# Performance work log

Measured on AMD Instinct MI355X. Metric: run time of the kernel, lower is better.

The kernel has to match this reference:

```python
import jax, jax.numpy as jnp
import numpy as np

B, T, C = 8, 1024, 1024
H, D = 16, 64  # num_heads, head_size

def setup_inputs() -> dict:
    key = jax.random.key(0)
    ks = jax.random.split(key, 6)
    s = C ** -0.5
    return {
        "x": jax.random.normal(ks[0], (B, T, C), dtype=jnp.float32),
        "Wq": jax.random.normal(ks[1], (H, C, D), dtype=jnp.float32) * s,
        "Wk": jax.random.normal(ks[2], (H, C, D), dtype=jnp.float32) * s,
        "Wv": jax.random.normal(ks[3], (H, C, D), dtype=jnp.float32) * s,
        "Wproj": jax.random.normal(ks[4], (H * D, C), dtype=jnp.float32) * ((H * D) ** -0.5),
        "bproj": jnp.zeros((C,), dtype=jnp.float32),
    }

def reference(x, Wq, Wk, Wv, Wproj, bproj):
    # per-head QKV projections, batched over heads via einsum (same math as looped heads)
    q = jnp.einsum('btc,hcd->bhtd', x, Wq)
    k = jnp.einsum('btc,hcd->bhtd', x, Wk)
    v = jnp.einsum('btc,hcd->bhtd', x, Wv)
    scale = D ** -0.5  # k.shape[-1]**-0.5 in original head
    scores = jnp.einsum('bhtd,bhsd->bhts', q, k) * scale  # [B,H,T,T]
    Tn = x.shape[1]
    causal = jnp.tril(jnp.ones((Tn, Tn), dtype=bool))
    scores = jnp.where(causal, scores, jnp.float32(-jnp.inf))
    att = jax.nn.softmax(scores, axis=-1)
    out = jnp.einsum('bhts,bhsd->bhtd', att, v)          # [B,H,T,D]
    out = out.transpose(0, 2, 1, 3).reshape(x.shape[0], Tn, H * D)  # concat heads
    return out @ Wproj + bproj  # dropout is identity at p=0.0
```

## Files before the change

### kernel.cpp

```cpp
#include <hip/hip_runtime.h>
#include <hip/hip_bf16.h>

#define B_ 8
#define T_ 1024
#define C_ 1024
#define H_ 16
#define D_ 64
#define QKVLD 3072

typedef short v4s __attribute__((ext_vector_type(4)));
typedef short v8s __attribute__((ext_vector_type(8)));
typedef float v4f __attribute__((ext_vector_type(4)));
typedef float v16f __attribute__((ext_vector_type(16)));

__device__ __forceinline__ unsigned short f2b(float f) {
    unsigned int u = __builtin_bit_cast(unsigned int, f);
    unsigned int lsb = (u >> 16) & 1u;
    u += 0x7fffu + lsb;
    return (unsigned short)(u >> 16);
}

__device__ __forceinline__ v4s pack4(float p0, float p1, float p2, float p3) {
    unsigned int a = (__builtin_bit_cast(unsigned int, p0) + 0x8000u) >> 16;
    unsigned int b = (__builtin_bit_cast(unsigned int, p1) + 0x8000u) & 0xFFFF0000u;
    unsigned int c = (__builtin_bit_cast(unsigned int, p2) + 0x8000u) >> 16;
    unsigned int d = (__builtin_bit_cast(unsigned int, p3) + 0x8000u) & 0xFFFF0000u;
    union { unsigned int u[2]; v4s v; } t;
    t.u[0] = a | b; t.u[1] = c | d;
    return t.v;
}

#define MFMA32(A, B, C) __builtin_amdgcn_mfma_f32_16x16x32_bf16(A, B, C, 0, 0, 0)
#define MFMA16(A, B, C) __builtin_amdgcn_mfma_f32_16x16x16bf16_1k(A, B, C, 0, 0, 0)

#define GLOAD16(gp, lp)                                                          \
    __builtin_amdgcn_global_load_lds(                                            \
        (const __attribute__((address_space(1))) unsigned int*)(gp),             \
        (__attribute__((address_space(3))) unsigned int*)(lp), 16, 0, 0)

__global__ void prep_kernel(const float* __restrict__ x, const float* __restrict__ Wq,
                            const float* __restrict__ Wk, const float* __restrict__ Wv,
                            const float* __restrict__ Wproj,
                            unsigned short* __restrict__ xb,
                            unsigned short* __restrict__ WqkvT,
                            unsigned short* __restrict__ WprojT) {
    __shared__ unsigned short t[64][65];
    int g = blockIdx.x;
    if (g < 8192) {
        int i = (g * 256 + (int)threadIdx.x) * 4;
        float4 v = *(const float4*)(x + i);
        ushort4 o;
        o.x = f2b(v.x); o.y = f2b(v.y); o.z = f2b(v.z); o.w = f2b(v.w);
        *(ushort4*)(xb + i) = o;
    } else if (g < 8192 + 768) {
        int idx = g - 8192;
        int z = idx >> 4;
        int h = z / 3, part = z % 3;
        const float* src = (part == 0 ? Wq : (part == 1 ? Wk : Wv)) + (size_t)h * C_ * D_;
        int c0 = (idx & 15) * 64;
        for (int i = threadIdx.x; i < 4096; i += 256) {
            int r = i >> 6, d = i & 63;
            t[d][r] = f2b(src[(size_t)(c0 + r) * D_ + d]);
        }
        __syncthreads();
        unsigned short* dst = WqkvT + (size_t)(part * 1024 + h * 64) * C_;
        for (int i = threadIdx.x; i < 4096; i += 256) {
            int d = i >> 6, r = i & 63;
            dst[(size_t)d * C_ + c0 + r] = t[d][r];
        }
    } else {
        int idx = g - 8960;
        int n0 = (idx & 15) * 64, k0 = (idx >> 4) * 64;
        for (int i = threadIdx.x; i < 4096; i += 256) {
            int r = i >> 6, c = i & 63;
            t[c][r] = f2b(Wproj[(size_t)(k0 + r) * C_ + n0 + c]);
        }
        __syncthreads();
        for (int i = threadIdx.x; i < 4096; i += 256) {
            int n = i >> 6, k = i & 63;
            WprojT[(size_t)(n0 + n) * 1024 + k0 + k] = t[n][k];
        }
    }
}

__global__ __launch_bounds__(256, 2) void gemm_qkv(const unsigned short* __restrict__ A,
                                                   const unsigned short* __restrict__ Bt,
                                                   unsigned short* __restrict__ Cout,
                                                   unsigned short* __restrict__ Vt,
                                                   int K, int ldc) {
    __shared__ unsigned short smem[24576];

    int tid = threadIdx.x;
    int lane = tid & 63, w = tid >> 6;
    int half = lane >> 5, l32 = lane & 31;
    int wm = w >> 1, wn = w & 1;
    int g = blockIdx.x;
    int xcd = g & 7;
    int bank = g >> 3;
    int j = g >> 4;

    if ((bank & 1) == 0) {
        constexpr int ABUF = 256 * 32;
        constexpr int BBUF = 128 * 32;
        unsigned short* lA0 = smem;
        unsigned short* lB0 = smem + 2 * ABUF;

        int m0 = (xcd * 4 + (j & 3)) * 256;
        int n0 = (j >> 2) * 128;

        const unsigned short* gA[4];
        int offA[4];
        #pragma unroll
        for (int jj = 0; jj < 4; jj++) {
            int c = jj * 256 + tid;
            int row = c >> 2;
            int col8 = ((c & 3) ^ ((row >> 1) & 3)) * 8;
            gA[jj] = A + (size_t)(m0 + row) * K + col8;
            offA[jj] = (jj * 256 + w * 64) * 16;
        }
        const unsigned short* gB[2];
        int offB[2];
        #pragma unroll
        for (int jj = 0; jj < 2; jj++) {
            int c = jj * 256 + tid;
            int row = c >> 2;
            int col8 = ((c & 3) ^ ((row >> 1) & 3)) * 8;
            gB[jj] = Bt + (size_t)(n0 + row) * K + col8;
            offB[jj] = (jj * 256 + w * 64) * 16;
        }

        int am[4], bn[2];
        #pragma unroll
        for (int mi = 0; mi < 4; mi++) am[mi] = wm * 128 + mi * 32 + l32;
        #pragma unroll
        for (int ni = 0; ni < 2; ni++) bn[ni] = wn * 64 + ni * 32 + l32;

        v16f acc[4][2];
        #pragma unroll
        for (int mi = 0; mi < 4; mi++)
            #pragma unroll
            for (int ni = 0; ni < 2; ni++)
                #pragma unroll
                for (int r = 0; r < 16; r++) acc[mi][ni][r] = 0.f;

        int ktiles = K >> 5;
        #pragma unroll
        for (int jj = 0; jj < 4; jj++) GLOAD16(gA[jj], (char*)lA0 + offA[jj]);
        #pragma unroll
        for (int jj = 0; jj < 2; jj++) GLOAD16(gB[jj], (char*)lB0 + offB[jj]);

        for (int it = 0; it < ktiles; it++) {
            int cur = it & 1, nxt = cur ^ 1;
            __asm__ volatile("s_waitcnt vmcnt(0)" ::: "memory");
            __asm__ volatile("s_barrier" ::: "memory");
            {
                int kn = (it + 1 < ktiles) ? (it + 1) * 32 : it * 32;
                #pragma unroll
                for (int jj = 0; jj < 4; jj++) GLOAD16(gA[jj] + kn, (char*)(lA0 + nxt * ABUF) + offA[jj]);
                #pragma unroll
                for (int jj = 0; jj < 2; jj++) GLOAD16(gB[jj] + kn, (char*)(lB0 + nxt * BBUF) + offB[jj]);
            }
            const unsigned short* bufA = lA0 + cur * ABUF;
            const unsigned short* bufB = lB0 + cur * BBUF;
            #pragma unroll
            for (int step = 0; step < 2; step++) {
                int gc = step * 2 + half;
                v8s af[4], bf[2];
                #pragma unroll
                for (int mi = 0; mi < 4; mi++)
                    af[mi] = *(const v8s*)&bufA[am[mi] * 32 + ((gc ^ ((am[mi] >> 1) & 3)) * 8)];
                #pragma unroll
                for (int ni = 0; ni < 2; ni++)
                    bf[ni] = *(const v8s*)&bufB[bn[ni] * 32 + ((gc ^ ((bn[ni] >> 1) & 3)) * 8)];
                #pragma unroll
                for (int mi = 0; mi < 4; mi++)
                    #pragma unroll
                    for (int ni = 0; ni < 2; ni++)
                        acc[mi][ni] = __builtin_amdgcn_mfma_f32_32x32x16_bf16(af[mi], bf[ni], acc[mi][ni], 0, 0, 0);
            }
        }
        float scl = (n0 >= 1024) ? 0.125f : 1.0f;
        #pragma unroll
        for (int mi = 0; mi < 4; mi++) {
            #pragma unroll
            for (int ni = 0; ni < 2; ni++) {
                int col = n0 + wn * 64 + ni * 32 + l32;
                #pragma unroll
                for (int r = 0; r < 16; r++) {
                    int row = m0 + wm * 128 + mi * 32 + (r & 3) + 8 * (r >> 2) + 4 * half;
                    Cout[(size_t)row * ldc + col] = f2b(acc[mi][ni][r] * scl);
                }
            }
        }
    } else {
        constexpr int ABUF = 128 * 32;
        constexpr int BBUF = 128 * 32;
        unsigned short* lA = smem;
        unsigned short* lB = smem + 3 * ABUF;

        const unsigned short* Bv = Bt + (size_t)2048 * K;
        int m0 = (xcd * 8 + (j & 7)) * 128;
        int n0 = (j >> 3) * 128;

        const unsigned short* gA[2];
        int offA[2];
        #pragma unroll
        for (int jj = 0; jj < 2; jj++) {
            int c = jj * 256 + tid;
            int row = c >> 2;
            int col8 = ((c & 3) ^ ((row >> 1) & 3)) * 8;
            gA[jj] = A + (size_t)(m0 + row) * K + col8;
            offA[jj] = (jj * 256 + w * 64) * 16;
        }
        const unsigned short* gB[2];
        int offB[2];
        #pragma unroll
        for (int jj = 0; jj < 2; jj++) {
            int c = jj * 256 + tid;
            int row = c >> 2;
            int col8 = ((c & 3) ^ ((row >> 1) & 3)) * 8;
            gB[jj] = Bv + (size_t)(n0 + row) * K + col8;
            offB[jj] = (jj * 256 + w * 64) * 16;
        }

        int am[2], bn[2];
        #pragma unroll
        for (int mi = 0; mi < 2; mi++) am[mi] = wm * 64 + mi * 32 + l32;
        #pragma unroll
        for (int ni = 0; ni < 2; ni++) bn[ni] = wn * 64 + ni * 32 + l32;

        v16f acc[2][2];
        #pragma unroll
        for (int mi = 0; mi < 2; mi++)
            #pragma unroll
            for (int ni = 0; ni < 2; ni++)
                #pragma unroll
                for (int r = 0; r < 16; r++) acc[mi][ni][r] = 0.f;

        int kt = K >> 5;
        #pragma unroll
        for (int jj = 0; jj < 2; jj++) GLOAD16(gA[jj], (char*)lA + offA[jj]);
        #pragma unroll
        for (int jj = 0; jj < 2; jj++) GLOAD16(gB[jj], (char*)lB + offB[jj]);
        #pragma unroll
        for (int jj = 0; jj < 2; jj++) GLOAD16(gA[jj] + 32, (char*)(lA + ABUF) + offA[jj]);
        #pragma unroll
        for (int jj = 0; jj < 2; jj++) GLOAD16(gB[jj] + 32, (char*)(lB + BBUF) + offB[jj]);

        int cur = 0;
        for (int it = 0; it < kt; it++) {
            int nx2 = cur + 2; if (nx2 >= 3) nx2 -= 3;
            __asm__ volatile("s_waitcnt vmcnt(4)" ::: "memory");
            __asm__ volatile("s_barrier" ::: "memory");
            {
                int kn = ((it + 2 < kt) ? it + 2 : kt - 1) << 5;
                #pragma unroll
                for (int jj = 0; jj < 2; jj++) GLOAD16(gA[jj] + kn, (char*)(lA + nx2 * ABUF) + offA[jj]);
                #pragma unroll
                for (int jj = 0; jj < 2; jj++) GLOAD16(gB[jj] + kn, (char*)(lB + nx2 * BBUF) + offB[jj]);
            }
            const unsigned short* bufA = lA + cur * ABUF;
            const unsigned short* bufB = lB + cur * BBUF;
            #pragma unroll
            for (int step = 0; step < 2; step++) {
                int gch = step * 2 + half;
                v8s af[2], bf[2];
                #pragma unroll
                for (int mi = 0; mi < 2; mi++)
                    af[mi] = *(const v8s*)&bufA[am[mi] * 32 + ((gch ^ ((am[mi] >> 1) & 3)) * 8)];
                #pragma unroll
                for (int ni = 0; ni < 2; ni++)
                    bf[ni] = *(const v8s*)&bufB[bn[ni] * 32 + ((gch ^ ((bn[ni] >> 1) & 3)) * 8)];
                #pragma unroll
                for (int mi = 0; mi < 2; mi++)
                    #pragma unroll
                    for (int ni = 0; ni < 2; ni++)
                        acc[mi][ni] = __builtin_amdgcn_mfma_f32_32x32x16_bf16(af[mi], bf[ni], acc[mi][ni], 0, 0, 0);
            }
            cur = cur + 1; if (cur >= 3) cur -= 3;
        }
        unsigned short* sT = lA;
        int bB = m0 >> 10;
        int t0 = m0 & 1023;
        #pragma unroll
        for (int p = 0; p < 2; p++) {
            __syncthreads();
            if (wn == p) {
                #pragma unroll
                for (int mi = 0; mi < 2; mi++)
                    #pragma unroll
                    for (int ni = 0; ni < 2; ni++) {
                        int cl = ni * 32 + l32;
                        #pragma unroll
                        for (int r = 0; r < 16; r++) {
                            int rowl = wm * 64 + mi * 32 + (r & 3) + 8 * (r >> 2) + 4 * half;
                            sT[cl * 136 + rowl] = f2b(acc[mi][ni][r]);
                        }
                    }
            }
            __syncthreads();
            #pragma unroll
            for (int jj = 0; jj < 4; jj++) {
                int c = jj * 256 + tid;
                int cl = c >> 4, ch = c & 15;
                int vcol = n0 + p * 64 + cl;
                int hh = vcol >> 6, dd = vcol & 63;
                *(v8s*)&Vt[(((size_t)bB * 16 + hh) * 64 + dd) * T_ + t0 + ch * 8] =
                    *(const v8s*)&sT[cl * 136 + ch * 8];
            }
        }
    }
}

__global__ __launch_bounds__(256, 3) void gemm_proj(const unsigned short* __restrict__ A,
                                                    const unsigned short* __restrict__ Bt,
                                                    float* __restrict__ Cout,
                                                    const float* __restrict__ bias,
                                                    int M, int N, int K) {
    constexpr int ABUF = 128 * 32;
    constexpr int BBUF = 128 * 32;
    __shared__ unsigned short lA[3 * ABUF];
    __shared__ unsigned short lB[3 * BBUF];

    int tid = threadIdx.x;
    int lane = tid & 63, w = tid >> 6;
    int half = lane >> 5, l32 = lane & 31;
    int wm = w >> 1, wn = w & 1;

    int g = blockIdx.x;
    int nbm = M / 128;
    int stripe = nbm >> 3;
    int xcd = g & 7, s = g >> 3;
    int m0 = (xcd * stripe + (s % stripe)) * 128;
    int n0 = (s / stripe) * 128;

    const unsigned short* gA[2];
    int offA[2];
    #pragma unroll
    for (int j = 0; j < 2; j++) {
        int c = j * 256 + tid;
        int row = c >> 2;
        int col8 = ((c & 3) ^ ((row >> 1) & 3)) * 8;
        gA[j] = A + (size_t)(m0 + row) * K + col8;
        offA[j] = (j * 256 + w * 64) * 16;
    }
    const unsigned short* gB[2];
    int offB[2];
    #pragma unroll
    for (int j = 0; j < 2; j++) {
        int c = j * 256 + tid;
        int row = c >> 2;
        int col8 = ((c & 3) ^ ((row >> 1) & 3)) * 8;
        gB[j] = Bt + (size_t)(n0 + row) * K + col8;
        offB[j] = (j * 256 + w * 64) * 16;
    }

    int am[2], bn[2];
    #pragma unroll
    for (int mi = 0; mi < 2; mi++) am[mi] = wm * 64 + mi * 32 + l32;
    #pragma unroll
    for (int ni = 0; ni < 2; ni++) bn[ni] = wn * 64 + ni * 32 + l32;

    v16f acc[2][2];
    #pragma unroll
    for (int mi = 0; mi < 2; mi++)
        #pragma unroll
        for (int ni = 0; ni < 2; ni++)
            #pragma unroll
            for (int r = 0; r < 16; r++) acc[mi][ni][r] = 0.f;

    int kt = K >> 5;
    #pragma unroll
    for (int j = 0; j < 2; j++) GLOAD16(gA[j], (char*)lA + offA[j]);
    #pragma unroll
    for (int j = 0; j < 2; j++) GLOAD16(gB[j], (char*)lB + offB[j]);
    #pragma unroll
    for (int j = 0; j < 2; j++) GLOAD16(gA[j] + 32, (char*)(lA + ABUF) + offA[j]);
    #pragma unroll
    for (int j = 0; j < 2; j++) GLOAD16(gB[j] + 32, (char*)(lB + BBUF) + offB[j]);

    int cur = 0;
    for (int it = 0; it < kt; it++) {
        int nx2 = cur + 2; if (nx2 >= 3) nx2 -= 3;
        __asm__ volatile("s_waitcnt vmcnt(4)" ::: "memory");
        __asm__ volatile("s_barrier" ::: "memory");
        {
            int kn = ((it + 2 < kt) ? it + 2 : kt - 1) << 5;
            #pragma unroll
            for (int j = 0; j < 2; j++) GLOAD16(gA[j] + kn, (char*)(lA + nx2 * ABUF) + offA[j]);
            #pragma unroll
            for (int j = 0; j < 2; j++) GLOAD16(gB[j] + kn, (char*)(lB + nx2 * BBUF) + offB[j]);
        }
        const unsigned short* bufA = lA + cur * ABUF;
        const unsigned short* bufB = lB + cur * BBUF;
        #pragma unroll
        for (int step = 0; step < 2; step++) {
            int gch = step * 2 + half;
            v8s af[2], bf[2];
            #pragma unroll
            for (int mi = 0; mi < 2; mi++)
                af[mi] = *(const v8s*)&bufA[am[mi] * 32 + ((gch ^ ((am[mi] >> 1) & 3)) * 8)];
            #pragma unroll
            for (int ni = 0; ni < 2; ni++)
                bf[ni] = *(const v8s*)&bufB[bn[ni] * 32 + ((gch ^ ((bn[ni] >> 1) & 3)) * 8)];
            #pragma unroll
            for (int mi = 0; mi < 2; mi++)
                #pragma unroll
                for (int ni = 0; ni < 2; ni++)
                    acc[mi][ni] = __builtin_amdgcn_mfma_f32_32x32x16_bf16(af[mi], bf[ni], acc[mi][ni], 0, 0, 0);
        }
        cur = cur + 1; if (cur >= 3) cur -= 3;
    }
    #pragma unroll
    for (int mi = 0; mi < 2; mi++) {
        #pragma unroll
        for (int ni = 0; ni < 2; ni++) {
            int col = n0 + wn * 64 + ni * 32 + l32;
            #pragma unroll
            for (int r = 0; r < 16; r++) {
                int row = m0 + wm * 64 + mi * 32 + (r & 3) + 8 * (r >> 2) + 4 * half;
                Cout[(size_t)row * N + col] = acc[mi][ni][r] + bias[col];
            }
        }
    }
}

__global__ __launch_bounds__(256) void attn_kernel(const unsigned short* __restrict__ QKV,
                                                   const unsigned short* __restrict__ Vt,
                                                   unsigned short* __restrict__ Ob) {
    int bh = blockIdx.x;
    int qt = 7 - blockIdx.y;
    int b = bh >> 4, h = bh & 15;
    int tid = threadIdx.x, lane = tid & 63, w = tid >> 6;
    int quad = lane >> 4, l16 = lane & 15;
    int qg0 = qt * 128 + w * 32;

    __shared__ unsigned short lK[2][2][64][32];
    __shared__ unsigned short lV[2][2][64][32];

    v8s aq[2][2];
    #pragma unroll
    for (int st = 0; st < 2; st++) {
        const unsigned short* qp = QKV + (size_t)(b * T_ + qg0 + st * 16 + l16) * QKVLD + h * 64;
        aq[st][0] = *(const v8s*)(qp + quad * 8);
        aq[st][1] = *(const v8s*)(qp + 32 + quad * 8);
    }

    const unsigned short* gK[2];
    const unsigned short* gV[2];
    int ldsOff[2];
    #pragma unroll
    for (int j = 0; j < 2; j++) {
        int c = j * 256 + tid;
        int halfp = c >> 8, row = (c >> 2) & 63;
        int col8 = ((c & 3) ^ ((row >> 1) & 3)) * 8;
        gK[j] = QKV + (size_t)(b * T_ + row) * QKVLD + 1024 + h * 64 + halfp * 32 + col8;
        gV[j] = Vt + ((size_t)bh * 64 + row) * T_ + halfp * 32 + col8;
        ldsOff[j] = (j * 256 + w * 64) * 16;
    }
    int rcol = (quad ^ ((l16 >> 1) & 3)) * 8;

    v4f accO[2][4];
    float lsum[2] = {0.f, 0.f};
    #pragma unroll
    for (int st = 0; st < 2; st++)
        #pragma unroll
        for (int i = 0; i < 4; i++) accO[st][i] = (v4f){0.f, 0.f, 0.f, 0.f};

    int ntiles = 2 * qt + 2;

    #pragma unroll
    for (int j = 0; j < 2; j++) GLOAD16(gK[j], (char*)&lK[0][0][0][0] + ldsOff[j]);
    #pragma unroll
    for (int j = 0; j < 2; j++) GLOAD16(gV[j], (char*)&lV[0][0][0][0] + ldsOff[j]);

    for (int it = 0; it < ntiles; it++) {
        int cur = it & 1, nxt = cur ^ 1;
        int s0 = it * 64;
        __asm__ volatile("s_waitcnt vmcnt(0)" ::: "memory");
        __asm__ volatile("s_barrier" ::: "memory");
        {
            int itn = (it + 1 < ntiles) ? it + 1 : it;
            size_t koff = (size_t)itn * 64 * QKVLD;
            #pragma unroll
            for (int j = 0; j < 2; j++)
                GLOAD16(gK[j] + koff, (char*)&lK[nxt][0][0][0] + ldsOff[j]);
            size_t voff = (size_t)itn * 64;
            #pragma unroll
            for (int j = 0; j < 2; j++)
                GLOAD16(gV[j] + voff, (char*)&lV[nxt][0][0][0] + ldsOff[j]);
        }
        bool diag = (it >= ntiles - 2);
        v4s pP[2][4];
        #pragma unroll
        for (int nt = 0; nt < 4; nt++) {
            v8s bk0 = *(const v8s*)&lK[cur][0][nt * 16 + l16][rcol];
            v8s bk1 = *(const v8s*)&lK[cur][1][nt * 16 + l16][rcol];
            #pragma unroll
            for (int st = 0; st < 2; st++) {
                v4f a = (v4f){0.f, 0.f, 0.f, 0.f};
                a = MFMA32(bk0, aq[st][0], a);
                a = MFMA32(bk1, aq[st][1], a);
                int qg = qg0 + st * 16 + l16;
                float p[4];
                #pragma unroll
                for (int r = 0; r < 4; r++) {
                    float e = __expf(a[r]);
                    if (diag) {
                        int sg = s0 + nt * 16 + quad * 4 + r;
                        e = (sg > qg) ? 0.f : e;
                    }
                    p[r] = e;
                    lsum[st] += e;
                }
                pP[st][nt] = pack4(p[0], p[1], p[2], p[3]);
            }
        }
        #pragma unroll
        for (int kb = 0; kb < 4; kb++) {
            int sc_ = kb >> 1;
            int ccg = (kb & 1) * 2 + (quad >> 1);
            #pragma unroll
            for (int dt = 0; dt < 4; dt++) {
                int d = dt * 16 + l16;
                int ccp = ccg ^ ((l16 >> 1) & 3);
                v4s bv = *(const v4s*)&lV[cur][sc_][d][ccp * 8 + (quad & 1) * 4];
                accO[0][dt] = MFMA16(pP[0][kb], bv, accO[0][dt]);
                accO[1][dt] = MFMA16(pP[1][kb], bv, accO[1][dt]);
            }
        }
    }
    #pragma unroll
    for (int st = 0; st < 2; st++) {
        float ls = lsum[st];
        ls += __shfl_xor(ls, 16, 64);
        ls += __shfl_xor(ls, 32, 64);
        #pragma unroll
        for (int r = 0; r < 4; r++) {
            float lq = __shfl(ls, quad * 4 + r, 64);
            float inv = 1.0f / lq;
            int q = qg0 + st * 16 + quad * 4 + r;
            #pragma unroll
            for (int dt = 0; dt < 4; dt++) {
                int d = dt * 16 + l16;
                Ob[(size_t)(b * T_ + q) * (H_ * D_) + h * 64 + d] = f2b(accO[st][dt][r] * inv);
            }
        }
    }
}

extern "C" void kernel_launch(void* const* d_in, const int* in_sizes, int n_in,
                              void* d_out, int out_size, void* d_ws, size_t ws_size,
                              hipStream_t stream) {
    const float* x     = (const float*)d_in[0];
    const float* Wq    = (const float*)d_in[1];
    const float* Wk    = (const float*)d_in[2];
    const float* Wv    = (const float*)d_in[3];
    const float* Wproj = (const float*)d_in[4];
    const float* bproj = (const float*)d_in[5];
    float* out = (float*)d_out;

    char* ws = (char*)d_ws;
    unsigned short* xb     = (unsigned short*)ws;
    unsigned short* WqkvT  = (unsigned short*)(ws + 16777216);
    unsigned short* WprojT = (unsigned short*)(ws + 23068672);
    unsigned short* QKV    = (unsigned short*)(ws + 25165824);
    unsigned short* Vt     = (unsigned short*)(ws + 75497472);
    unsigned short* Ob     = (unsigned short*)(ws + 92274688);

    prep_kernel<<<dim3(9216), dim3(256), 0, stream>>>(x, Wq, Wk, Wv, Wproj, xb, WqkvT, WprojT);
    gemm_qkv<<<dim3(1024), dim3(256), 0, stream>>>(xb, WqkvT, QKV, Vt, 1024, QKVLD);
    attn_kernel<<<dim3(128, 8), dim3(256), 0, stream>>>(QKV, Vt, Ob);
    gemm_proj<<<dim3(512), dim3(256), 0, stream>>>(Ob, WprojT, out, bproj, 8192, 1024, 1024);
}
```

Baseline: 230.3 us.

## Unify QKV GEMM onto uniform 128x128 triple-buffered tiles for all outputs

Replaces the split QKV GEMM, which used 256x128 double-buffered tiles for Q/K and 128x128 triple-buffered tiles for V, with a single 128x128 triple-buffered path for every output column block. The grid grows from 1024 to 1536 blocks and occupancy is raised to 3 blocks per CU. The aim is to cut branch divergence, deepen the prefetch pipeline and balance work across blocks. The cost is lower data reuse per tile for Q/K, since each A tile is now loaded for only 128 output columns, which raises global and LDS traffic.

```diff
diff --git a/kernel.cpp b/kernel.cpp
--- a/kernel.cpp
+++ b/kernel.cpp
@@ -83,205 +83,123 @@
     }
 }
 
-__global__ __launch_bounds__(256, 2) void gemm_qkv(const unsigned short* __restrict__ A,
+__global__ __launch_bounds__(256, 3) void gemm_qkv(const unsigned short* __restrict__ A,
                                                    const unsigned short* __restrict__ Bt,
                                                    unsigned short* __restrict__ Cout,
                                                    unsigned short* __restrict__ Vt,
                                                    int K, int ldc) {
-    __shared__ unsigned short smem[24576];
+    constexpr int ABUF = 128 * 32;
+    constexpr int BBUF = 128 * 32;
+    __shared__ unsigned short lA[3 * ABUF];
+    __shared__ unsigned short lB[3 * BBUF];
 
     int tid = threadIdx.x;
     int lane = tid & 63, w = tid >> 6;
     int half = lane >> 5, l32 = lane & 31;
     int wm = w >> 1, wn = w & 1;
+
     int g = blockIdx.x;
-    int xcd = g & 7;
-    int bank = g >> 3;
-    int j = g >> 4;
-
-    if ((bank & 1) == 0) {
-        constexpr int ABUF = 256 * 32;
-        constexpr int BBUF = 128 * 32;
-        unsigned short* lA0 = smem;
-        unsigned short* lB0 = smem + 2 * ABUF;
-
-        int m0 = (xcd * 4 + (j & 3)) * 256;
-        int n0 = (j >> 2) * 128;
-
-        const unsigned short* gA[4];
-        int offA[4];
-        #pragma unroll
-        for (int jj = 0; jj < 4; jj++) {
-            int c = jj * 256 + tid;
-            int row = c >> 2;
-            int col8 = ((c & 3) ^ ((row >> 1) & 3)) * 8;
-            gA[jj] = A + (size_t)(m0 + row) * K + col8;
-            offA[jj] = (jj * 256 + w * 64) * 16;
-        }
-        const unsigned short* gB[2];
-        int offB[2];
-        #pragma unroll
-        for (int jj = 0; jj < 2; jj++) {
-            int c = jj * 256 + tid;
-            int row = c >> 2;
-            int col8 = ((c & 3) ^ ((row >> 1) & 3)) * 8;
-            gB[jj] = Bt + (size_t)(n0 + row) * K + col8;
-            offB[jj] = (jj * 256 + w * 64) * 16;
-        }
-
-        int am[4], bn[2];
-        #pragma unroll
-        for (int mi = 0; mi < 4; mi++) am[mi] = wm * 128 + mi * 32 + l32;
-        #pragma unroll
-        for (int ni = 0; ni < 2; ni++) bn[ni] = wn * 64 + ni * 32 + l32;
-
-        v16f acc[4][2];
-        #pragma unroll
-        for (int mi = 0; mi < 4; mi++)
+    int xcd = g & 7, s = g >> 3;
+    int m0 = (xcd * 8 + (s & 7)) * 128;
+    int n0 = (s >> 3) * 128;
+
+    const unsigned short* gA[2];
+    int offA[2];
+    #pragma unroll
+    for (int j = 0; j < 2; j++) {
+        int c = j * 256 + tid;
+        int row = c >> 2;
+        int col8 = ((c & 3) ^ ((row >> 1) & 3)) * 8;
+        gA[j] = A + (size_t)(m0 + row) * K + col8;
+        offA[j] = (j * 256 + w * 64) * 16;
+    }
+    const unsigned short* gB[2];
+    int offB[2];
+    #pragma unroll
+    for (int j = 0; j < 2; j++) {
+        int c = j * 256 + tid;
+        int row = c >> 2;
+        int col8 = ((c & 3) ^ ((row >> 1) & 3)) * 8;
+        gB[j] = Bt + (size_t)(n0 + row) * K + col8;
+        offB[j] = (j * 256 + w * 64) * 16;
+    }
+
+    int am[2], bn[2];
+    #pragma unroll
+    for (int mi = 0; mi < 2; mi++) am[mi] = wm * 64 + mi * 32 + l32;
+    #pragma unroll
+    for (int ni = 0; ni < 2; ni++) bn[ni] = wn * 64 + ni * 32 + l32;
+
+    v16f acc[2][2];
+    #pragma unroll
+    for (int mi = 0; mi < 2; mi++)
+        #pragma unroll
+        for (int ni = 0; ni < 2; ni++)
+            #pragma unroll
+            for (int r = 0; r < 16; r++) acc[mi][ni][r] = 0.f;
+
+    int kt = K >> 5;
+    #pragma unroll
+    for (int j = 0; j < 2; j++) GLOAD16(gA[j], (char*)lA + offA[j]);
+    #pragma unroll
+    for (int j = 0; j < 2; j++) GLOAD16(gB[j], (char*)lB + offB[j]);
+    #pragma unroll
+    for (int j = 0; j < 2; j++) GLOAD16(gA[j] + 32, (char*)(lA + ABUF) + offA[j]);
+    #pragma unroll
+    for (int j = 0; j < 2; j++) GLOAD16(gB[j] + 32, (char*)(lB + BBUF) + offB[j]);
+
+    int cur = 0;
+    for (int it = 0; it < kt; it++) {
+        int nx2 = cur + 2; if (nx2 >= 3) nx2 -= 3;
+        __asm__ volatile("s_waitcnt vmcnt(4)" ::: "memory");
+        __asm__ volatile("s_barrier" ::: "memory");
+        {
+            int kn = ((it + 2 < kt) ? it + 2 : kt - 1) << 5;
+            #pragma unroll
+            for (int j = 0; j < 2; j++) GLOAD16(gA[j] + kn, (char*)(lA + nx2 * ABUF) + offA[j]);
+            #pragma unroll
+            for (int j = 0; j < 2; j++) GLOAD16(gB[j] + kn, (char*)(lB + nx2 * BBUF) + offB[j]);
+        }
+        const unsigned short* bufA = lA + cur * ABUF;
+        const unsigned short* bufB = lB + cur * BBUF;
+        #pragma unroll
+        for (int step = 0; step < 2; step++) {
+            int gch = step * 2 + half;
+            v8s af[2], bf[2];
+            #pragma unroll
+            for (int mi = 0; mi < 2; mi++)
+                af[mi] = *(const v8s*)&bufA[am[mi] * 32 + ((gch ^ ((am[mi] >> 1) & 3)) * 8)];
             #pragma unroll
             for (int ni = 0; ni < 2; ni++)
-                #pragma unroll
-                for (int r = 0; r < 16; r++) acc[mi][ni][r] = 0.f;
-
-        int ktiles = K >> 5;
-        #pragma unroll
-        for (int jj = 0; jj < 4; jj++) GLOAD16(gA[jj], (char*)lA0 + offA[jj]);
-        #pragma unroll
-        for (int jj = 0; jj < 2; jj++) GLOAD16(gB[jj], (char*)lB0 + offB[jj]);
-
-        for (int it = 0; it < ktiles; it++) {
-            int cur = it & 1, nxt = cur ^ 1;
-            __asm__ volatile("s_waitcnt vmcnt(0)" ::: "memory");
-            __asm__ volatile("s_barrier" ::: "memory");
-            {
-                int kn = (it + 1 < ktiles) ? (it + 1) * 32 : it * 32;
-                #pragma unroll
-                for (int jj = 0; jj < 4; jj++) GLOAD16(gA[jj] + kn, (char*)(lA0 + nxt * ABUF) + offA[jj]);
-                #pragma unroll
-                for (int jj = 0; jj < 2; jj++) GLOAD16(gB[jj] + kn, (char*)(lB0 + nxt * BBUF) + offB[jj]);
-            }
-            const unsigned short* bufA = lA0 + cur * ABUF;
-            const unsigned short* bufB = lB0 + cur * BBUF;
-            #pragma unroll
-            for (int step = 0; step < 2; step++) {
-                int gc = step * 2 + half;
-                v8s af[4], bf[2];
-                #pragma unroll
-                for (int mi = 0; mi < 4; mi++)
-                    af[mi] = *(const v8s*)&bufA[am[mi] * 32 + ((gc ^ ((am[mi] >> 1) & 3)) * 8)];
+                bf[ni] = *(const v8s*)&bufB[bn[ni] * 32 + ((gch ^ ((bn[ni] >> 1) & 3)) * 8)];
+            #pragma unroll
+            for (int mi = 0; mi < 2; mi++)
                 #pragma unroll
                 for (int ni = 0; ni < 2; ni++)
-                    bf[ni] = *(const v8s*)&bufB[bn[ni] * 32 + ((gc ^ ((bn[ni] >> 1) & 3)) * 8)];
-                #pragma unroll
-                for (int mi = 0; mi < 4; mi++)
-                    #pragma unroll
-                    for (int ni = 0; ni < 2; ni++)
-                        acc[mi][ni] = __builtin_amdgcn_mfma_f32_32x32x16_bf16(af[mi], bf[ni], acc[mi][ni], 0, 0, 0);
-            }
-        }
+                    acc[mi][ni] = __builtin_amdgcn_mfma_f32_32x32x16_bf16(af[mi], bf[ni], acc[mi][ni], 0, 0, 0);
+        }
+        cur = cur + 1; if (cur >= 3) cur -= 3;
+    }
+
+    if (n0 < 2048) {
         float scl = (n0 >= 1024) ? 0.125f : 1.0f;
         #pragma unroll
-        for (int mi = 0; mi < 4; mi++) {
+        for (int mi = 0; mi < 2; mi++) {
             #pragma unroll
             for (int ni = 0; ni < 2; ni++) {
                 int col = n0 + wn * 64 + ni * 32 + l32;
                 #pragma unroll
                 for (int r = 0; r < 16; r++) {
-                    int row = m0 + wm * 128 + mi * 32 + (r & 3) + 8 * (r >> 2) + 4 * half;
+                    int row = m0 + wm * 64 + mi * 32 + (r & 3) + 8 * (r >> 2) + 4 * half;
                     Cout[(size_t)row * ldc + col] = f2b(acc[mi][ni][r] * scl);
                 }
             }
         }
     } else {
-        constexpr int ABUF = 128 * 32;
-        constexpr int BBUF = 128 * 32;
-        unsigned short* lA = smem;
-        unsigned short* lB = smem + 3 * ABUF;
-
-        const unsigned short* Bv = Bt + (size_t)2048 * K;
-        int m0 = (xcd * 8 + (j & 7)) * 128;
-        int n0 = (j >> 3) * 128;
-
-        const unsigned short* gA[2];
-        int offA[2];
-        #pragma unroll
-        for (int jj = 0; jj < 2; jj++) {
-            int c = jj * 256 + tid;
-            int row = c >> 2;
-            int col8 = ((c & 3) ^ ((row >> 1) & 3)) * 8;
-            gA[jj] = A + (size_t)(m0 + row) * K + col8;
-            offA[jj] = (jj * 256 + w * 64) * 16;
-        }
-        const unsigned short* gB[2];
-        int offB[2];
-        #pragma unroll
-        for (int jj = 0; jj < 2; jj++) {
-            int c = jj * 256 + tid;
-            int row = c >> 2;
-            int col8 = ((c & 3) ^ ((row >> 1) & 3)) * 8;
-            gB[jj] = Bv + (size_t)(n0 + row) * K + col8;
-            offB[jj] = (jj * 256 + w * 64) * 16;
-        }
-
-        int am[2], bn[2];
-        #pragma unroll
-        for (int mi = 0; mi < 2; mi++) am[mi] = wm * 64 + mi * 32 + l32;
-        #pragma unroll
-        for (int ni = 0; ni < 2; ni++) bn[ni] = wn * 64 + ni * 32 + l32;
-
-        v16f acc[2][2];
-        #pragma unroll
-        for (int mi = 0; mi < 2; mi++)
-            #pragma unroll
-            for (int ni = 0; ni < 2; ni++)
-                #pragma unroll
-                for (int r = 0; r < 16; r++) acc[mi][ni][r] = 0.f;
-
-        int kt = K >> 5;
-        #pragma unroll
-        for (int jj = 0; jj < 2; jj++) GLOAD16(gA[jj], (char*)lA + offA[jj]);
-        #pragma unroll
-        for (int jj = 0; jj < 2; jj++) GLOAD16(gB[jj], (char*)lB + offB[jj]);
-        #pragma unroll
-        for (int jj = 0; jj < 2; jj++) GLOAD16(gA[jj] + 32, (char*)(lA + ABUF) + offA[jj]);
-        #pragma unroll
-        for (int jj = 0; jj < 2; jj++) GLOAD16(gB[jj] + 32, (char*)(lB + BBUF) + offB[jj]);
-
-        int cur = 0;
-        for (int it = 0; it < kt; it++) {
-            int nx2 = cur + 2; if (nx2 >= 3) nx2 -= 3;
-            __asm__ volatile("s_waitcnt vmcnt(4)" ::: "memory");
-            __asm__ volatile("s_barrier" ::: "memory");
-            {
-                int kn = ((it + 2 < kt) ? it + 2 : kt - 1) << 5;
-                #pragma unroll
-                for (int jj = 0; jj < 2; jj++) GLOAD16(gA[jj] + kn, (char*)(lA + nx2 * ABUF) + offA[jj]);
-                #pragma unroll
-                for (int jj = 0; jj < 2; jj++) GLOAD16(gB[jj] + kn, (char*)(lB + nx2 * BBUF) + offB[jj]);
-            }
-            const unsigned short* bufA = lA + cur * ABUF;
-            const unsigned short* bufB = lB + cur * BBUF;
-            #pragma unroll
-            for (int step = 0; step < 2; step++) {
-                int gch = step * 2 + half;
-                v8s af[2], bf[2];
-                #pragma unroll
-                for (int mi = 0; mi < 2; mi++)
-                    af[mi] = *(const v8s*)&bufA[am[mi] * 32 + ((gch ^ ((am[mi] >> 1) & 3)) * 8)];
-                #pragma unroll
-                for (int ni = 0; ni < 2; ni++)
-                    bf[ni] = *(const v8s*)&bufB[bn[ni] * 32 + ((gch ^ ((bn[ni] >> 1) & 3)) * 8)];
-                #pragma unroll
-                for (int mi = 0; mi < 2; mi++)
-                    #pragma unroll
-                    for (int ni = 0; ni < 2; ni++)
-                        acc[mi][ni] = __builtin_amdgcn_mfma_f32_32x32x16_bf16(af[mi], bf[ni], acc[mi][ni], 0, 0, 0);
-            }
-            cur = cur + 1; if (cur >= 3) cur -= 3;
-        }
         unsigned short* sT = lA;
         int bB = m0 >> 10;
         int t0 = m0 & 1023;
+        int nv = n0 - 2048;
         #pragma unroll
         for (int p = 0; p < 2; p++) {
             __syncthreads();
@@ -300,10 +218,10 @@
             }
             __syncthreads();
             #pragma unroll
-            for (int jj = 0; jj < 4; jj++) {
-                int c = jj * 256 + tid;
+            for (int j = 0; j < 4; j++) {
+                int c = j * 256 + tid;
                 int cl = c >> 4, ch = c & 15;
-                int vcol = n0 + p * 64 + cl;
+                int vcol = nv + p * 64 + cl;
                 int hh = vcol >> 6, dd = vcol & 63;
                 *(v8s*)&Vt[(((size_t)bB * 16 + hh) * 64 + dd) * T_ + t0 + ch * 8] =
                     *(const v8s*)&sT[cl * 136 + ch * 8];
@@ -569,7 +487,7 @@
     unsigned short* Ob     = (unsigned short*)(ws + 92274688);
 
     prep_kernel<<<dim3(9216), dim3(256), 0, stream>>>(x, Wq, Wk, Wv, Wproj, xb, WqkvT, WprojT);
-    gemm_qkv<<<dim3(1024), dim3(256), 0, stream>>>(xb, WqkvT, QKV, Vt, 1024, QKVLD);
+    gemm_qkv<<<dim3(1536), dim3(256), 0, stream>>>(xb, WqkvT, QKV, Vt, 1024, QKVLD);
     attn_kernel<<<dim3(128, 8), dim3(256), 0, stream>>>(QKV, Vt, Ob);
     gemm_proj<<<dim3(512), dim3(256), 0, stream>>>(Ob, WprojT, out, bproj, 8192, 1024, 1024);
 }
```

Result: no change. 231.3 us (+0.4%).
